# Optimization experiments

Measured on AMD Instinct MI355X. Metric: run time of the kernel, lower is better.

The kernel has to match this reference:

```python
import jax, jax.numpy as jnp
import numpy as np
from jax import lax

# Quantization bit-widths per the module: QuantAct(16) on input,
# QuantConv2d(precision[0]=8), QuantAct(precision[0]+3=11) after relu1,
# QuantLinear(precision[1]=8).
INPUT_BIT = 16
CONV_W_BIT = 8
RELU_BIT = 11
DENSE_W_BIT = 8
EPS = 1e-8


def round_ste(x):
    # straight-through estimator rounding (HAWQ SymmetricQuantFunction)
    return x + lax.stop_gradient(jnp.round(x) - x)


def quant_act(x, bit):
    """Per-tensor symmetric dynamic activation quantization (HAWQ QuantAct).
    Returns fake-quantized x and its scaling factor."""
    n = 2 ** (bit - 1) - 1
    scale = lax.stop_gradient(jnp.maximum(jnp.max(jnp.abs(x)), EPS) / n)
    x_q = jnp.clip(round_ste(x / scale), -n, n) * scale
    return x_q, scale


def quant_weight(w, bit):
    """Per-output-channel symmetric weight quantization. w: [out, ...].
    Returns integer-valued weights and per-channel scale [out]."""
    n = 2 ** (bit - 1) - 1
    absmax = jnp.max(jnp.abs(w.reshape(w.shape[0], -1)), axis=1)
    sf = lax.stop_gradient(jnp.maximum(absmax, EPS) / n)
    bshape = (w.shape[0],) + (1,) * (w.ndim - 1)
    w_int = jnp.clip(round_ste(w / sf.reshape(bshape)), -n, n)
    return w_int, sf


def quant_conv2d(x, p_sf, w, b, bit, stride, pad):
    w_int, w_sf = quant_weight(w, bit)          # [O,I,kh,kw], [O]
    x_int = x / p_sf                            # integer-valued activations
    out_int = lax.conv_general_dilated(
        x_int, w_int, window_strides=(stride, stride),
        padding=((pad, pad), (pad, pad)),
        dimension_numbers=("NCHW", "OIHW", "NCHW"))
    bias_sf = p_sf * w_sf                       # [O]
    b_int = round_ste(b / bias_sf)
    out = (out_int + b_int[None, :, None, None]) * bias_sf[None, :, None, None]
    return out, w_sf


def quant_linear(x, p_sf, w, b, bit):
    w_int, w_sf = quant_weight(w, bit)          # [O,I], [O]
    x_int = x / p_sf
    bias_sf = p_sf * w_sf                       # [O]
    b_int = round_ste(b / bias_sf)
    out = (jnp.einsum("bi,oi->bo", x_int, w_int) + b_int[None, :]) * bias_sf[None, :]
    return out


def setup_inputs() -> dict:
    key = jax.random.key(0)
    k1, k2, k3, k4, k5 = jax.random.split(key, 5)
    B, Cin, H, W = 256, 3, 64, 64
    Cout, K = 64, 3
    Fin, Fout = Cout * 32 * 32, 256  # stride-2 conv -> 32x32 spatial
    x = jax.random.normal(k1, (B, Cin, H, W), dtype=jnp.float32)
    conv_w = jax.random.normal(k2, (Cout, Cin, K, K), dtype=jnp.float32) * 0.1
    conv_b = jax.random.normal(k3, (Cout,), dtype=jnp.float32) * 0.01
    dense_w = jax.random.normal(k4, (Fout, Fin), dtype=jnp.float32) * 0.02
    dense_b = jax.random.normal(k5, (Fout,), dtype=jnp.float32) * 0.01
    return {"x": x, "conv_w": conv_w, "conv_b": conv_b,
            "dense_w": dense_w, "dense_b": dense_b}


def reference(x, conv_w, conv_b, dense_w, dense_b):
    # x, p_sf = quant_input(x)
    xq, p_sf = quant_act(x, INPUT_BIT)
    # x, w_sf = conv(x, p_sf)
    h, w_sf = quant_conv2d(xq, p_sf, conv_w, conv_b, CONV_W_BIT, stride=2, pad=1)
    # relu1
    h = jax.nn.relu(h)
    # x, p_sf = quant_relu(x, p_sf, w_sf)  (requantize at relu_bit)
    h, p_sf = quant_act(h, RELU_BIT)
    # flatten
    h = h.reshape(h.shape[0], -1)
    # relu2(enc_dense(x, p_sf))
    out = jax.nn.relu(quant_linear(h, p_sf, dense_w, dense_b, DENSE_W_BIT))
    return out
```

## Files before the change

### kernel.cpp

```cpp
#include <hip/hip_runtime.h>
#include <hip/hip_fp16.h>
#include <cstdint>

#define B_   256
#define CIN  3
#define HW_  64
#define COUT 64
#define FIN  65536
#define FOUT 256

#define ACC_F    0
#define SC_F     65536
#define XPART_F  65552
#define WPART_F  66064
#define CSF_F    67088
#define CWINT_F  67152
#define H16_BYTE (512*1024)
#define WQ_BYTE  (H16_BYTE + 256ll*FIN*2)

typedef _Float16 half8  __attribute__((ext_vector_type(8)));
typedef _Float16 half4v __attribute__((ext_vector_type(4)));
typedef float    floatx4 __attribute__((ext_vector_type(4)));
typedef unsigned short u16;
typedef unsigned int uint_;

__device__ inline float blockMax(float v) {
    #pragma unroll
    for (int off = 32; off; off >>= 1) v = fmaxf(v, __shfl_down(v, off));
    __shared__ float sm[8];
    const int lane = threadIdx.x & 63, w = threadIdx.x >> 6;
    if (lane == 0) sm[w] = v;
    __syncthreads();
    float m = sm[0];
    const int nw = blockDim.x >> 6;
    for (int i = 1; i < nw; i++) m = fmaxf(m, sm[i]);
    return m;
}

__global__ __launch_bounds__(256) void k_stats(const float* __restrict__ x,
                                               const float* __restrict__ dw,
                                               const float* __restrict__ cw,
                                               float* __restrict__ ws) {
    const int b = blockIdx.x;
    const int t = threadIdx.x;
    if (b < 512) {
        const float4* x4 = (const float4*)x;
        float m = 0.f;
        for (int i = b * 256 + t; i < (B_ * CIN * HW_ * HW_) / 4; i += 512 * 256) {
            float4 v = x4[i];
            m = fmaxf(m, fmaxf(fmaxf(fabsf(v.x), fabsf(v.y)), fmaxf(fabsf(v.z), fabsf(v.w))));
        }
        float bm = blockMax(m);
        if (t == 0) ws[XPART_F + b] = bm;
    } else if (b < 1536) {
        const int b2 = b - 512;
        const int row = b2 >> 2, q = b2 & 3;
        const float4* r = (const float4*)(dw + (size_t)row * FIN) + q * 4096;
        float m = 0.f;
        for (int i = t; i < 4096; i += 256) {
            float4 v = r[i];
            m = fmaxf(m, fmaxf(fmaxf(fabsf(v.x), fabsf(v.y)), fmaxf(fabsf(v.z), fabsf(v.w))));
        }
        float bm = blockMax(m);
        if (t == 0) ws[WPART_F + b2] = bm;
    } else if (b == 1536) {
        if (t == 64) ((unsigned*)ws)[SC_F + 1] = 0u;
        if (t < 64) {
            const int o = t;
            float wv[27];
            float m = 0.f;
            #pragma unroll
            for (int i = 0; i < 27; i++) { wv[i] = cw[o * 27 + i]; m = fmaxf(m, fabsf(wv[i])); }
            const float sf = fmaxf(m, 1e-8f) / 127.0f;
            #pragma unroll
            for (int i = 0; i < 27; i++)
                ws[CWINT_F + o * 27 + i] = fminf(127.f, fmaxf(-127.f, rintf(wv[i] / sf)));
            ws[CSF_F + o] = sf;
        }
    } else {
        ws[ACC_F + (b - 1537) * 256 + t] = 0.f;
    }
}

__global__ __launch_bounds__(256) void k_conv(const float* __restrict__ x,
                                              const float* __restrict__ dw,
                                              const float* __restrict__ cb,
                                              const float* __restrict__ ws,
                                              u16* __restrict__ h16,
                                              signed char* __restrict__ wq,
                                              unsigned* __restrict__ maxh) {
    const int t = threadIdx.x;

    __shared__ float s_bsf[64], s_bint[64];
    __shared__ float xt[27 * 68];

    float pm = fmaxf(ws[XPART_F + t], ws[XPART_F + 256 + t]);
    pm = blockMax(pm);
    const float p_sf = fmaxf(pm, 1e-8f) / 32767.0f;
    const float inv_p = 1.0f / p_sf;
    if (t < 64) {
        const float bsf = p_sf * ws[CSF_F + t];
        s_bsf[t]  = bsf;
        s_bint[t] = rintf(cb[t] / bsf);
    }

    const int b   = blockIdx.x >> 3;
    const int oyt = (blockIdx.x & 7) * 4;
    const float* xb = x + (size_t)b * (CIN * HW_ * HW_);

    for (int i = t; i < 432; i += 256) {
        const int lrow = i >> 4, c4 = i & 15;
        const int ci = lrow / 9, lr = lrow - ci * 9;
        const int iy = 2 * oyt - 1 + lr;
        float4 v = make_float4(0.f, 0.f, 0.f, 0.f);
        if ((unsigned)iy < 64u) v = *(const float4*)(xb + (ci * HW_ + iy) * HW_ + c4 * 4);
        float* d = &xt[lrow * 68 + 1 + c4 * 4];
        d[0] = rintf(v.x * inv_p);
        d[1] = rintf(v.y * inv_p);
        d[2] = rintf(v.z * inv_p);
        d[3] = rintf(v.w * inv_p);
    }
    if (t < 27) xt[t * 68] = 0.f;
    else if (t < 54) xt[(t - 27) * 68 + 65] = 0.f;
    __syncthreads();

    const int ox = t & 31;
    const int ch = __builtin_amdgcn_readfirstlane((t >> 6) & 1);
    const int dy = ((t >> 7) << 1) + ((t >> 5) & 1);
    const int oy = oyt + dy;

    float xs[27];
    #pragma unroll
    for (int ci = 0; ci < 3; ci++)
        #pragma unroll
        for (int ky = 0; ky < 3; ky++) {
            const float* rowp = &xt[(ci * 9 + 2 * dy + ky) * 68 + 2 * ox];
            float a0 = rowp[0], a1 = rowp[1], a2 = rowp[2];
            asm volatile("" : "+v"(a0), "+v"(a1), "+v"(a2));
            xs[ci * 9 + ky * 3 + 0] = a0;
            xs[ci * 9 + ky * 3 + 1] = a1;
            xs[ci * 9 + ky * 3 + 2] = a2;
        }

    const float* wr = ws + CWINT_F + ch * (32 * 27);
    float mx = 0.f;
    u16* outp = h16 + (size_t)b * FIN + (size_t)ch * 32 * 1024 + oy * 32 + ox;

#define EMIT(cc, aa) { const int co_ = ch * 32 + (cc); \
    float h_ = ((aa) + s_bint[co_]) * s_bsf[co_]; \
    h_ = fmaxf(h_, 0.f); mx = fmaxf(mx, h_); \
    outp[(size_t)(cc) * 1024] = __half_as_ushort(__float2half(h_)); }

    float wA[27], wB[27];
    #pragma unroll
    for (int k = 0; k < 27; k++) wA[k] = wr[k];
    #pragma unroll
    for (int c = 0; c < 32; c += 2) {
        #pragma unroll
        for (int k = 0; k < 27; k++) wB[k] = wr[(c + 1) * 27 + k];
        float a = 0.f;
        #pragma unroll
        for (int k = 0; k < 27; k++) a = fmaf(xs[k], wA[k], a);
        EMIT(c, a);
        if (c + 2 < 32) {
            #pragma unroll
            for (int k = 0; k < 27; k++) wA[k] = wr[(c + 2) * 27 + k];
        }
        float a2 = 0.f;
        #pragma unroll
        for (int k = 0; k < 27; k++) a2 = fmaf(xs[k], wB[k], a2);
        EMIT(c + 1, a2);
    }
#undef EMIT
    float bm = blockMax(mx);
    if (t == 0) atomicMax(maxh, __float_as_uint(bm));

    {
        const int row = blockIdx.x >> 3;
        const int e8  = blockIdx.x & 7;
        const float* wp = ws + WPART_F + row * 4;
        const float am = fmaxf(fmaxf(wp[0], wp[1]), fmaxf(wp[2], wp[3]));
        const float inv = 127.0f / fmaxf(am, 1e-8f);
        const float4* r4 = (const float4*)(dw + (size_t)row * FIN) + e8 * 2048;
        uint_* wrow = (uint_*)(wq + (size_t)row * FIN) + e8 * 2048;
        for (int i = t; i < 2048; i += 256) {
            float4 v = r4[i];
            int q0 = __float2int_rn(v.x * inv);
            int q1 = __float2int_rn(v.y * inv);
            int q2 = __float2int_rn(v.z * inv);
            int q3 = __float2int_rn(v.w * inv);
            wrow[i] = (uint_)(q0 & 255) | ((uint_)(q1 & 255) << 8) |
                      ((uint_)(q2 & 255) << 16) | ((uint_)(q3 & 255) << 24);
        }
    }
}

__device__ __forceinline__ half8 cvt_b8(uint_ lo, uint_ hi) {
    half8 h;
    h[0] = (_Float16)(float)(int)(signed char)(lo);
    h[1] = (_Float16)(float)(int)(signed char)(lo >> 8);
    h[2] = (_Float16)(float)(int)(signed char)(lo >> 16);
    h[3] = (_Float16)(float)(int)(signed char)(lo >> 24);
    h[4] = (_Float16)(float)(int)(signed char)(hi);
    h[5] = (_Float16)(float)(int)(signed char)(hi >> 8);
    h[6] = (_Float16)(float)(int)(signed char)(hi >> 16);
    h[7] = (_Float16)(float)(int)(signed char)(hi >> 24);
    return h;
}

__global__ __launch_bounds__(256) void k_gemm(const u16* __restrict__ h16,
                                              const signed char* __restrict__ wq,
                                              const float* __restrict__ ws,
                                              float* __restrict__ accb) {
    __shared__ __align__(16) _Float16 As[128][72];
    __shared__ __align__(16) _Float16 Bs[128][72];

    const int tid = threadIdx.x;
    const int tm  = (blockIdx.x >> 1) * 128;
    const int tn  = (blockIdx.x & 1) * 128;
    const int k0  = blockIdx.y * 1024;

    const float max_h  = __uint_as_float(((const unsigned*)ws)[SC_F + 1]);
    const float p2     = fmaxf(max_h, 1e-8f) / 1023.0f;
    const float inv_p2 = 1.0f / p2;

    floatx4 acc[4][4];
    const floatx4 zz = {0.f, 0.f, 0.f, 0.f};
    #pragma unroll
    for (int i = 0; i < 4; i++)
        #pragma unroll
        for (int j = 0; j < 4; j++) acc[i][j] = zz;

    const int wv = tid >> 6, lane = tid & 63;
    const int wm = (wv >> 1) * 64, wn = (wv & 1) * 64;
    const int lm = lane & 15, quad = lane >> 4;

    const int arow = tid >> 3, acol = tid & 7;
    const int brow = tid >> 1, bq   = (tid & 1) * 32;
    const u16* abase = h16 + (size_t)(tm + arow) * FIN + k0 + acol * 8;
    const signed char* bbase = wq + (size_t)(tn + brow) * FIN + k0 + bq;

#define LOADA(dst, kk) { _Pragma("unroll") \
    for (int r = 0; r < 4; r++) \
        dst[r] = *(const half8*)(abase + (size_t)r * 32 * FIN + (kk) * 64); }
#define LOADB(dst, kk) { const uint4* p_ = (const uint4*)(bbase + (kk) * 64); \
    dst[0] = p_[0]; dst[1] = p_[1]; }
#define STAGEA(src) { _Pragma("unroll") \
    for (int r = 0; r < 4; r++) { half8 qv; _Pragma("unroll") \
        for (int j = 0; j < 8; j++) { float f_ = (float)src[r][j]; \
            qv[j] = (_Float16)fminf(1023.f, rintf(f_ * inv_p2)); } \
        *(half8*)&As[arow + r * 32][acol * 8] = qv; } }
#define STAGEB(src) { _Pragma("unroll") \
    for (int u = 0; u < 2; u++) { uint4 wd_ = src[u]; \
        *(half8*)&Bs[brow][bq + u * 16 + 0] = cvt_b8(wd_.x, wd_.y); \
        *(half8*)&Bs[brow][bq + u * 16 + 8] = cvt_b8(wd_.z, wd_.w); } }
#define BARRIER() do { asm volatile("s_waitcnt lgkmcnt(0)" ::: "memory"); \
    __builtin_amdgcn_s_barrier(); } while (0)
#define MFMA_PHASE() { _Pragma("unroll") \
    for (int ks = 0; ks < 2; ks++) { half8 af[4], bf[4]; _Pragma("unroll") \
        for (int mi = 0; mi < 4; mi++) \
            af[mi] = *(const half8*)&As[wm + mi * 16 + lm][ks * 32 + quad * 8]; \
        _Pragma("unroll") \
        for (int ni = 0; ni < 4; ni++) \
            bf[ni] = *(const half8*)&Bs[wn + ni * 16 + lm][ks * 32 + quad * 8]; \
        _Pragma("unroll") \
        for (int mi = 0; mi < 4; mi++) _Pragma("unroll") \
            for (int ni = 0; ni < 4; ni++) \
                acc[mi][ni] = __builtin_amdgcn_mfma_f32_16x16x32_f16(af[mi], bf[ni], acc[mi][ni], 0, 0, 0); } }

    half8 a0[4], a1[4];
    uint4 b0[2], b1[2];

    LOADA(a0, 0); LOADB(b0, 0);
    LOADA(a1, 1); LOADB(b1, 1);

    for (int it = 0; it < 8; ++it) {
        STAGEA(a0); STAGEB(b0);
        if (it < 7) { LOADA(a0, 2 * it + 2); LOADB(b0, 2 * it + 2); }
        BARRIER();
        MFMA_PHASE();
        BARRIER();
        STAGEA(a1); STAGEB(b1);
        if (it < 7) { LOADA(a1, 2 * it + 3); LOADB(b1, 2 * it + 3); }
        BARRIER();
        MFMA_PHASE();
        BARRIER();
    }

    #pragma unroll
    for (int mi = 0; mi < 4; mi++)
        #pragma unroll
        for (int ni = 0; ni < 4; ni++)
            #pragma unroll
            for (int r = 0; r < 4; r++) {
                const int row = tm + wm + mi * 16 + quad * 4 + r;
                const int col = tn + wn + ni * 16 + lm;
                atomicAdd(accb + row * FOUT + col, acc[mi][ni][r]);
            }
#undef LOADA
#undef LOADB
#undef STAGEA
#undef STAGEB
#undef BARRIER
#undef MFMA_PHASE
}

__global__ void k_epi(const float* __restrict__ accb, const float* __restrict__ db,
                      const float* __restrict__ ws, float* __restrict__ out) {
    const int idx = blockIdx.x * 256 + threadIdx.x;
    const int n = idx & 255;
    const float max_h = __uint_as_float(((const unsigned*)ws)[SC_F + 1]);
    const float p2 = fmaxf(max_h, 1e-8f) / 1023.0f;
    const float* wp = ws + WPART_F + (size_t)n * 4;
    const float am = fmaxf(fmaxf(fmaxf(wp[0], wp[1]), fmaxf(wp[2], wp[3])), 1e-8f);
    const float wsf = am / 127.0f;
    const float bsf = p2 * wsf;
    const float bint = rintf(db[n] / bsf);
    out[idx] = fmaxf(0.f, (accb[idx] + bint) * bsf);
}

extern "C" void kernel_launch(void* const* d_in, const int* in_sizes, int n_in,
                              void* d_out, int out_size, void* d_ws, size_t ws_size,
                              hipStream_t stream) {
    (void)in_sizes; (void)n_in; (void)out_size; (void)ws_size;
    const float* x  = (const float*)d_in[0];
    const float* cw = (const float*)d_in[1];
    const float* cb = (const float*)d_in[2];
    const float* dw = (const float*)d_in[3];
    const float* db = (const float*)d_in[4];
    float* out = (float*)d_out;
    float* ws  = (float*)d_ws;
    u16* h16   = (u16*)((char*)d_ws + H16_BYTE);
    signed char* wq = (signed char*)d_ws + WQ_BYTE;
    float* accb = ws + ACC_F;
    unsigned* maxh = (unsigned*)ws + SC_F + 1;

    k_stats<<<1793, 256, 0, stream>>>(x, dw, cw, ws);
    k_conv<<<2048, 256, 0, stream>>>(x, dw, cb, ws, h16, wq, maxh);
    k_gemm<<<dim3(4, 64), 256, 0, stream>>>(h16, wq, ws, accb);
    k_epi<<<256, 256, 0, stream>>>(accb, db, ws, out);
}
```

Measured before the change: 189.4 us.

## Fuse epilogue into GEMM kernel via grid-wide atomic barrier

Removes the separate epilogue kernel launch by appending the bias/scale/ReLU epilogue to the split-K GEMM kernel. A global atomic ticket counter, reset in the stats kernel, acts as a grid barrier so every block waits until all 256 blocks have finished their atomic accumulations. After that, each block writes one 256-element row of the output. This saves one launch but relies on all 256 blocks being co-resident, and blocks spin-wait at the end.

```diff
diff --git a/kernel.cpp b/kernel.cpp
--- a/kernel.cpp
+++ b/kernel.cpp
@@ -65,6 +65,7 @@
         if (t == 0) ws[WPART_F + b2] = bm;
     } else if (b == 1536) {
         if (t == 64) ((unsigned*)ws)[SC_F + 1] = 0u;
+        if (t == 65) ((unsigned*)ws)[SC_F + 3] = 0u;
         if (t < 64) {
             const int o = t;
             float wv[27];
@@ -211,7 +212,10 @@
 __global__ __launch_bounds__(256) void k_gemm(const u16* __restrict__ h16,
                                               const signed char* __restrict__ wq,
                                               const float* __restrict__ ws,
-                                              float* __restrict__ accb) {
+                                              float* __restrict__ accb,
+                                              const float* __restrict__ db,
+                                              float* __restrict__ out,
+                                              unsigned* __restrict__ tick) {
     __shared__ __align__(16) _Float16 As[128][72];
     __shared__ __align__(16) _Float16 Bs[128][72];
 
@@ -303,20 +307,25 @@
 #undef STAGEB
 #undef BARRIER
 #undef MFMA_PHASE
-}
-
-__global__ void k_epi(const float* __restrict__ accb, const float* __restrict__ db,
-                      const float* __restrict__ ws, float* __restrict__ out) {
-    const int idx = blockIdx.x * 256 + threadIdx.x;
-    const int n = idx & 255;
-    const float max_h = __uint_as_float(((const unsigned*)ws)[SC_F + 1]);
-    const float p2 = fmaxf(max_h, 1e-8f) / 1023.0f;
-    const float* wp = ws + WPART_F + (size_t)n * 4;
-    const float am = fmaxf(fmaxf(fmaxf(wp[0], wp[1]), fmaxf(wp[2], wp[3])), 1e-8f);
-    const float wsf = am / 127.0f;
-    const float bsf = p2 * wsf;
-    const float bint = rintf(db[n] / bsf);
-    out[idx] = fmaxf(0.f, (accb[idx] + bint) * bsf);
+
+    __threadfence();
+    if (tid == 0) {
+        atomicAdd(tick, 1u);
+        while (atomicAdd(tick, 0u) < 256u) __builtin_amdgcn_s_sleep(8);
+    }
+    __syncthreads();
+    __threadfence();
+
+    {
+        const int fbid = blockIdx.y * 4 + blockIdx.x;
+        const int idx = fbid * 256 + tid;
+        const int n = tid;
+        const float* wp = ws + WPART_F + (size_t)n * 4;
+        const float am = fmaxf(fmaxf(fmaxf(wp[0], wp[1]), fmaxf(wp[2], wp[3])), 1e-8f);
+        const float bsf = p2 * (am / 127.0f);
+        const float bint = rintf(db[n] / bsf);
+        out[idx] = fmaxf(0.f, (accb[idx] + bint) * bsf);
+    }
 }
 
 extern "C" void kernel_launch(void* const* d_in, const int* in_sizes, int n_in,
@@ -334,9 +343,9 @@
     signed char* wq = (signed char*)d_ws + WQ_BYTE;
     float* accb = ws + ACC_F;
     unsigned* maxh = (unsigned*)ws + SC_F + 1;
+    unsigned* tick = (unsigned*)ws + SC_F + 3;
 
     k_stats<<<1793, 256, 0, stream>>>(x, dw, cw, ws);
     k_conv<<<2048, 256, 0, stream>>>(x, dw, cb, ws, h16, wq, maxh);
-    k_gemm<<<dim3(4, 64), 256, 0, stream>>>(h16, wq, ws, accb);
-    k_epi<<<256, 256, 0, stream>>>(accb, db, ws, out);
-}
+    k_gemm<<<dim3(4, 64), 256, 0, stream>>>(h16, wq, ws, accb, db, out, tick);
+}
```

Result: slower. 225.4 us (+19.0%).
